# Kernel optimization log

Measured on AMD Instinct MI355X. Metric: run time of the kernel, lower is better.

Reference implementation:

```python
import math
import jax, jax.numpy as jnp
import numpy as np

B, T, E, H, D = 4, 2048, 1024, 16, 64


def make_pe(max_len, d_model):
    pos = np.arange(max_len, dtype=np.float32)[:, None]
    div = np.exp(np.arange(0, d_model, 2, dtype=np.float32) * (-math.log(10000.0) / d_model))
    pe = np.zeros((max_len, d_model), dtype=np.float32)
    pe[:, 0::2] = np.sin(pos * div)
    pe[:, 1::2] = np.cos(pos * div)
    return jnp.asarray(pe)


def _rel_shift(x):
    # x: [T, K, B, H] -- Transformer-XL relative shift
    Tq, K, b, h = x.shape
    zp = jnp.zeros((Tq, 1, b, h), x.dtype)
    xp = jnp.concatenate([zp, x], axis=1).reshape(K + 1, Tq, b, h)
    return xp[1:].reshape(Tq, K, b, h)


def setup_inputs() -> dict:
    key = jax.random.key(0)
    ks = jax.random.split(key, 7)
    word_embedding = jax.random.normal(ks[0], (B, T, E), dtype=jnp.float32)
    lens = jax.random.randint(ks[1], (B,), 128, T + 1)  # >=128 so no empty softmax rows
    # torch Linear weights are [out, in]
    Wqkv = jax.random.normal(ks[2], (3 * H * D, E), dtype=jnp.float32) * (1.0 / math.sqrt(E))
    Wpos = jax.random.normal(ks[3], (H * D, E), dtype=jnp.float32) * (1.0 / math.sqrt(E))
    Wout = jax.random.normal(ks[4], (E, H * D), dtype=jnp.float32) * (1.0 / math.sqrt(H * D))
    bound = math.sqrt(6.0 / (H + D))  # xavier_uniform on [H, D]
    r_w_bias = jax.random.uniform(ks[5], (H, D), minval=-bound, maxval=bound, dtype=jnp.float32)
    r_r_bias = jax.random.uniform(ks[6], (H, D), minval=-bound, maxval=bound, dtype=jnp.float32)
    return {"word_embedding": word_embedding, "lens": lens, "Wqkv": Wqkv,
            "Wpos": Wpos, "Wout": Wout, "r_w_bias": r_w_bias, "r_r_bias": r_r_bias}


def reference(word_embedding, lens, Wqkv, Wpos, Wout, r_w_bias, r_r_bias):
    scale = 1.0 / math.sqrt(D)
    we = jnp.transpose(word_embedding, (1, 0, 2))  # [T, B, E]
    K = T  # mems=None
    pe = make_pe(K, E)  # [K, E], constant buffer

    heads = jnp.einsum('tbe,fe->tbf', we, Wqkv)  # [T, B, 3HD]
    q, k, v = jnp.split(heads, 3, axis=-1)
    q = q.reshape(T, B, H, D)
    k = k.reshape(K, B, H, D)
    v = v.reshape(K, B, H, D)
    Rk = (pe @ Wpos.T).reshape(K, H, D)  # [K, H, D]

    AC = jnp.einsum('ibnd,jbnd->ijbn', q + r_w_bias, k)   # [T, K, B, H]
    BD = _rel_shift(jnp.einsum('ibnd,jnd->ijbn', q + r_r_bias, Rk))
    score = (AC + BD) * scale

    # mask: key position j invalid if j >= lens[b]
    mask = jnp.arange(K)[:, None] >= lens[None, :]       # [K, B]
    score = jnp.where(mask[None, :, :, None], -1e30, score)
    prob = jax.nn.softmax(score, axis=1)

    vec = jnp.einsum('ijbn,jbnd->ibnd', prob, v).reshape(T, B, H * D)
    out = jnp.einsum('tbf,ef->tbe', vec, Wout)           # [T, B, E]
    return jnp.transpose(out, (1, 0, 2))                 # [B, T, E]
```

## Files before the change

kernel.cpp:

```cpp
#include <hip/hip_runtime.h>
#include <hip/hip_bf16.h>
#include <math.h>
#include <stdint.h>

constexpr int Bc  = 4;
constexpr int Tc  = 2048;
constexpr int Ec  = 1024;
constexpr int Hc  = 16;
constexpr int Dc  = 64;
constexpr int HDc = Hc * Dc;
constexpr int Kc  = Tc;
constexpr float SCL2E = 0.18033688011112042f;

typedef __bf16 bf16;
typedef __attribute__((ext_vector_type(8))) __bf16 bf16x8;
typedef __attribute__((ext_vector_type(4))) __bf16 bf16x4;
typedef __attribute__((ext_vector_type(4))) float f32x4;
typedef __attribute__((ext_vector_type(4))) _Float16 f16x4;

__device__ __forceinline__ void gload16(const bf16* gp, bf16* lp) {
  __builtin_amdgcn_global_load_lds(
      (const __attribute__((address_space(1))) void*)gp,
      (__attribute__((address_space(3))) void*)lp, 16, 0, 0);
}

__global__ __launch_bounds__(256) void split_kernel(
    const float* __restrict__ src, bf16* __restrict__ hi,
    bf16* __restrict__ lo, int n) {
  int i = (blockIdx.x * 256 + threadIdx.x) * 4;
  if (i >= n) return;
  float4 v = *(const float4*)(src + i);
  bf16 h0 = (bf16)v.x, h1 = (bf16)v.y, h2 = (bf16)v.z, h3 = (bf16)v.w;
  bf16x4 H = {h0, h1, h2, h3};
  bf16x4 L = {(bf16)(v.x - (float)h0), (bf16)(v.y - (float)h1),
              (bf16)(v.z - (float)h2), (bf16)(v.w - (float)h3)};
  *(bf16x4*)(hi + i) = H;
  *(bf16x4*)(lo + i) = L;
}

__global__ __launch_bounds__(256) void round_kernel(
    const float* __restrict__ src, bf16* __restrict__ dst, int n) {
  int i = (blockIdx.x * 256 + threadIdx.x) * 4;
  if (i >= n) return;
  float4 v = *(const float4*)(src + i);
  bf16x4 H = {(bf16)v.x, (bf16)v.y, (bf16)v.z, (bf16)v.w};
  *(bf16x4*)(dst + i) = H;
}

__global__ __launch_bounds__(256) void pe_kernel(bf16* __restrict__ peH) {
  int idx = blockIdx.x * blockDim.x + threadIdx.x;
  if (idx >= Kc * (Ec / 2)) return;
  int r = idx / (Ec / 2);
  int i = idx % (Ec / 2);
  float div = __expf((float)i * -0.017988946039015984f);
  float ang = (float)r * div;
  size_t o = (size_t)r * Ec + 2 * i;
  peH[o]     = (bf16)sinf(ang);
  peH[o + 1] = (bf16)cosf(ang);
}

template <int EPI, int SPLIT>
__global__ __launch_bounds__(256) void gemm_mfma(
    const bf16* __restrict__ Ah_g, const bf16* __restrict__ Al_g,
    const bf16* __restrict__ Bh_g, const bf16* __restrict__ Bl_g,
    void* __restrict__ o0, void* __restrict__ o1,
    void* __restrict__ o2, void* __restrict__ o3,
    const float* __restrict__ rwb, const float* __restrict__ rrb,
    int Kd) {
  const int bn = blockIdx.x * 128, bm = blockIdx.y * 128;
  const int tid = threadIdx.x, wv = tid >> 6, lane = tid & 63;
  const int wm = wv >> 1, wn = wv & 1;
  const int g = lane >> 4, laneL = lane & 15;

  __shared__ bf16 lds[(SPLIT ? 4 : 2) * 128 * 64];
  bf16* Ah = lds;
  bf16* Al = lds + 8192;
  bf16* Bh = lds + (SPLIT ? 16384 : 8192);
  bf16* Bl = lds + 24576;

  f32x4 acc[4][4];
#pragma unroll
  for (int fi = 0; fi < 4; fi++)
#pragma unroll
    for (int fj = 0; fj < 4; fj++) acc[fi][fj] = (f32x4){0.f, 0.f, 0.f, 0.f};

  const int rb  = lane >> 3;
  const int cb8 = ((lane & 7) ^ rb) * 8;
  const bf16* Abase_h = Ah_g + (size_t)bm * Kd;
  const bf16* Abase_l = SPLIT ? Al_g + (size_t)bm * Kd : nullptr;
  const bf16* Bbase_h = Bh_g + (size_t)bn * Kd;
  const bf16* Bbase_l = SPLIT ? Bl_g + (size_t)bn * Kd : nullptr;

  for (int k0 = 0; k0 < Kd; k0 += 64) {
    __syncthreads();
#pragma unroll
    for (int t = 0; t < 4; t++) {
      int r = t * 32 + wv * 8 + rb;
      size_t go = (size_t)r * Kd + k0 + cb8;
      int lo_ = (t * 32 + wv * 8) * 64;
      gload16(Abase_h + go, Ah + lo_);
      gload16(Bbase_h + go, Bh + lo_);
      if (SPLIT) {
        gload16(Abase_l + go, Al + lo_);
        gload16(Bbase_l + go, Bl + lo_);
      }
    }
    __syncthreads();
#pragma unroll
    for (int kk = 0; kk < 2; kk++) {
      bf16x8 afh[4], afl[4], bfh[4], bfl[4];
#pragma unroll
      for (int fi = 0; fi < 4; fi++) {
        int row = wm * 64 + fi * 16 + laneL;
        int off = row * 64 + (((kk * 4 + g) ^ (row & 7)) * 8);
        afh[fi] = *(const bf16x8*)(Ah + off);
        if (SPLIT) afl[fi] = *(const bf16x8*)(Al + off);
      }
#pragma unroll
      for (int fj = 0; fj < 4; fj++) {
        int row = wn * 64 + fj * 16 + laneL;
        int off = row * 64 + (((kk * 4 + g) ^ (row & 7)) * 8);
        bfh[fj] = *(const bf16x8*)(Bh + off);
        if (SPLIT) bfl[fj] = *(const bf16x8*)(Bl + off);
      }
#pragma unroll
      for (int fi = 0; fi < 4; fi++)
#pragma unroll
        for (int fj = 0; fj < 4; fj++) {
          acc[fi][fj] = __builtin_amdgcn_mfma_f32_16x16x32_bf16(afh[fi], bfh[fj], acc[fi][fj], 0, 0, 0);
          if (SPLIT) {
            acc[fi][fj] = __builtin_amdgcn_mfma_f32_16x16x32_bf16(afh[fi], bfl[fj], acc[fi][fj], 0, 0, 0);
            acc[fi][fj] = __builtin_amdgcn_mfma_f32_16x16x32_bf16(afl[fi], bfh[fj], acc[fi][fj], 0, 0, 0);
          }
        }
    }
  }

#pragma unroll
  for (int fi = 0; fi < 4; fi++) {
#pragma unroll
    for (int fj = 0; fj < 4; fj++) {
      int n = bn + wn * 64 + fj * 16 + laneL;
      int sec = n >> 10, f = n & 1023, hh = f >> 6, d = f & 63;
      float rw = 0.f, rr = 0.f;
      if (EPI == 0 && sec == 0) { rw = rwb[f]; rr = rrb[f]; }
#pragma unroll
      for (int rg = 0; rg < 4; rg++) {
        int m = bm + wm * 64 + fi * 16 + g * 4 + rg;
        float cv = acc[fi][fj][rg];
        if (EPI == 0) {
          int bb = m >> 11, t = m & 2047;
          if (sec == 0) {
            size_t o = (((size_t)(bb * Hc + hh)) * Tc + t) * 64 + d;
            ((bf16*)o0)[o] = (bf16)((cv + rw) * SCL2E);
            ((bf16*)o1)[o] = (bf16)((cv + rr) * SCL2E);
          } else if (sec == 1) {
            ((bf16*)o2)[(((size_t)(bb * Hc + hh)) * Tc + t) * 64 + d] = (bf16)cv;
          } else {
            ((bf16*)o3)[(((size_t)(bb * Hc + hh)) * 64 + d) * Tc + t] = (bf16)cv;
          }
        } else if (EPI == 1) {
          ((bf16*)o0)[((size_t)(n >> 6) * Kc + m) * 64 + (n & 63)] = (bf16)cv;
        } else {
          ((float*)o0)[(size_t)m * 1024 + n] = cv;
        }
      }
    }
  }
}

__global__ __launch_bounds__(256, 2) void attn_mfma(
    const bf16* __restrict__ qw, const bf16* __restrict__ qr,
    const bf16* __restrict__ kbuf, const bf16* __restrict__ vT,
    const bf16* __restrict__ Rk, const int* __restrict__ lens,
    bf16* __restrict__ vecH, bf16* __restrict__ vecL) {
  const int bid = blockIdx.x;
  const int h  = (bid & 7) * 2 + ((bid >> 3) & 1);
  const int i0 = ((bid >> 4) & 31) * 64;
  const int b  = bid >> 9;
  const int tid = threadIdx.x, wv = tid >> 6, lane = tid & 63;
  const int g = lane >> 4, laneL = lane & 15;
  const int len = lens[b];

  __shared__ __attribute__((aligned(16))) _Float16 Gs[4][16 * 84];
  __shared__ bf16 Kst[2][64 * 64];
  __shared__ bf16 Vst[2][64 * 64];

  const size_t bh = (size_t)(b * Hc + h) * Tc * 64;
  const bf16* qwB = qw   + bh;
  const bf16* qrB = qr   + bh;
  const bf16* kB  = kbuf + bh;
  const bf16* vTB = vT   + bh;
  const bf16* RkB = Rk   + (size_t)h * Kc * 64;

  const int myrow  = i0 + wv * 16 + laneL;
  const int myrow2 = (myrow + 1 < Tc) ? myrow + 1 : Tc - 1;
  bf16x8 bqw[2], bq1[2], bq2[2];
#pragma unroll
  for (int kk = 0; kk < 2; kk++) {
    bqw[kk] = *(const bf16x8*)(qwB + (size_t)myrow  * 64 + kk * 32 + g * 8);
    bq1[kk] = *(const bf16x8*)(qrB + (size_t)myrow  * 64 + kk * 32 + g * 8);
    bq2[kk] = *(const bf16x8*)(qrB + (size_t)myrow2 * 64 + kk * 32 + g * 8);
  }

  float m_ = -1e30f, l_ = 0.f;
  f32x4 O[4];
#pragma unroll
  for (int nf = 0; nf < 4; nf++) O[nf] = (f32x4){0.f, 0.f, 0.f, 0.f};

  _Float16* Gp = &Gs[wv][0];
  bf16*     Pp = (bf16*)&Gs[wv][0];
  const int pswz = (laneL & 7) << 3;

  auto stage = [&](int buf, int j0n) __attribute__((always_inline)) {
#pragma unroll
    for (int t = 0; t < 2; t++) {
      const int r0  = wv * 16 + t * 8;
      const int row = r0 + (lane >> 3);
      const int c8  = (lane & 7) ^ ((lane >> 3) & 7);
      gload16(kB  + (size_t)(j0n + row) * 64 + c8 * 8, &Kst[buf][r0 * 64]);
      gload16(vTB + (size_t)row * Tc + j0n + c8 * 8,   &Vst[buf][r0 * 64]);
    }
  };

  auto issue_rk = [&](bf16x8 (&rf)[10], int j0n) __attribute__((always_inline)) {
    const int cn = i0 - j0n;
    const int pb = (cn >= 0 ? Tc - 16 - cn : -cn - 17) - wv * 16;
#pragma unroll
    for (int mf = 0; mf < 5; mf++) {
      int p = pb + mf * 16 + laneL;
      p = p < 0 ? 0 : (p > Kc - 1 ? Kc - 1 : p);
#pragma unroll
      for (int kk = 0; kk < 2; kk++)
        rf[mf * 2 + kk] = *(const bf16x8*)(RkB + (size_t)p * 64 + kk * 32 + g * 8);
    }
  };

  auto compute_tile = [&](int cur, int j0c, const bf16x8 (&rf)[10])
      __attribute__((always_inline)) {
    const int c = i0 - j0c;
    const int swz8 = laneL & 7;

    f32x4 ST[4];
    __builtin_amdgcn_s_setprio(1);
#pragma unroll
    for (int nf = 0; nf < 4; nf++) {
      f32x4 acc = (f32x4){0.f, 0.f, 0.f, 0.f};
#pragma unroll
      for (int kk = 0; kk < 2; kk++) {
        bf16x8 bk = *(const bf16x8*)(&Kst[cur][(nf * 16 + laneL) * 64 + (((kk * 4 + g) ^ swz8) * 8)]);
        acc = __builtin_amdgcn_mfma_f32_16x16x32_bf16(bk, bqw[kk], acc, 0, 0, 0);
      }
      ST[nf] = acc;
    }
    __builtin_amdgcn_s_setprio(0);

    const int iic  = wv * 16 + laneL + c;
    const int colb = laneL * 84 + 15 - laneL;
    float P_[4][4];

    if (c > 0) {
      __builtin_amdgcn_s_setprio(1);
#pragma unroll
      for (int mf = 0; mf < 5; mf++) {
        f32x4 acc = (f32x4){0.f, 0.f, 0.f, 0.f};
#pragma unroll
        for (int kk = 0; kk < 2; kk++)
          acc = __builtin_amdgcn_mfma_f32_16x16x32_bf16(rf[mf * 2 + kk], bq1[kk], acc, 0, 0, 0);
        f16x4 gv = {(_Float16)acc[0], (_Float16)acc[1], (_Float16)acc[2], (_Float16)acc[3]};
        *(f16x4*)(Gp + laneL * 84 + mf * 16 + g * 4) = gv;
      }
      __builtin_amdgcn_s_setprio(0);
#pragma unroll
      for (int nf = 0; nf < 4; nf++)
#pragma unroll
        for (int r = 0; r < 4; r++)
          P_[nf][r] = (float)Gp[colb + nf * 16 + g * 4 + r];
    } else if (c < 0) {
      __builtin_amdgcn_s_setprio(1);
#pragma unroll
      for (int mf = 0; mf < 5; mf++) {
        f32x4 acc = (f32x4){0.f, 0.f, 0.f, 0.f};
#pragma unroll
        for (int kk = 0; kk < 2; kk++)
          acc = __builtin_amdgcn_mfma_f32_16x16x32_bf16(rf[mf * 2 + kk], bq2[kk], acc, 0, 0, 0);
        f16x4 gv = {(_Float16)acc[0], (_Float16)acc[1], (_Float16)acc[2], (_Float16)acc[3]};
        *(f16x4*)(Gp + laneL * 84 + mf * 16 + g * 4) = gv;
      }
      __builtin_amdgcn_s_setprio(0);
#pragma unroll
      for (int nf = 0; nf < 4; nf++)
#pragma unroll
        for (int r = 0; r < 4; r++) {
          const int jj = nf * 16 + g * 4 + r;
          float g2v = (float)Gp[colb + jj];
          P_[nf][r] = (jj == iic + 1) ? 0.f : g2v;
        }
    } else {
      __builtin_amdgcn_s_setprio(1);
#pragma unroll
      for (int mf = 0; mf < 5; mf++) {
        f32x4 acc = (f32x4){0.f, 0.f, 0.f, 0.f};
#pragma unroll
        for (int kk = 0; kk < 2; kk++)
          acc = __builtin_amdgcn_mfma_f32_16x16x32_bf16(rf[mf * 2 + kk], bq1[kk], acc, 0, 0, 0);
        f16x4 gv = {(_Float16)acc[0], (_Float16)acc[1], (_Float16)acc[2], (_Float16)acc[3]};
        *(f16x4*)(Gp + laneL * 84 + mf * 16 + g * 4) = gv;
      }
      __builtin_amdgcn_s_setprio(0);
#pragma unroll
      for (int nf = 0; nf < 4; nf++)
#pragma unroll
        for (int r = 0; r < 4; r++)
          P_[nf][r] = (float)Gp[colb + nf * 16 + g * 4 + r];
      const int pb = -17 - wv * 16;
      __builtin_amdgcn_s_setprio(1);
#pragma unroll
      for (int mf = 0; mf < 5; mf++) {
        int p = pb + mf * 16 + laneL;
        p = p < 0 ? 0 : (p > Kc - 1 ? Kc - 1 : p);
        f32x4 acc = (f32x4){0.f, 0.f, 0.f, 0.f};
#pragma unroll
        for (int kk = 0; kk < 2; kk++) {
          bf16x8 ark = *(const bf16x8*)(RkB + (size_t)p * 64 + kk * 32 + g * 8);
          acc = __builtin_amdgcn_mfma_f32_16x16x32_bf16(ark, bq2[kk], acc, 0, 0, 0);
        }
        f16x4 gv = {(_Float16)acc[0], (_Float16)acc[1], (_Float16)acc[2], (_Float16)acc[3]};
        *(f16x4*)(Gp + laneL * 84 + mf * 16 + g * 4) = gv;
      }
      __builtin_amdgcn_s_setprio(0);
#pragma unroll
      for (int nf = 0; nf < 4; nf++)
#pragma unroll
        for (int r = 0; r < 4; r++) {
          const int jj = nf * 16 + g * 4 + r;
          float g2v = (float)Gp[colb + jj];
          P_[nf][r] = (jj <= iic) ? P_[nf][r] : ((jj == iic + 1) ? 0.f : g2v);
        }
    }

    float mx = -1e30f;
#pragma unroll
    for (int nf = 0; nf < 4; nf++)
#pragma unroll
      for (int r = 0; r < 4; r++) {
        float s = ST[nf][r] + P_[nf][r];
        P_[nf][r] = s;
        mx = fmaxf(mx, s);
      }
    if (j0c + 64 > len) {
#pragma unroll
      for (int nf = 0; nf < 4; nf++)
#pragma unroll
        for (int r = 0; r < 4; r++) {
          const int jj = nf * 16 + g * 4 + r;
          if (j0c + jj >= len) P_[nf][r] = -1e30f;
        }
      mx = -1e30f;
#pragma unroll
      for (int nf = 0; nf < 4; nf++)
#pragma unroll
        for (int r = 0; r < 4; r++) mx = fmaxf(mx, P_[nf][r]);
    }
    mx = fmaxf(mx, __shfl_xor(mx, 16));
    mx = fmaxf(mx, __shfl_xor(mx, 32));
    const float mnew = fmaxf(m_, mx);
    const bool norescale = __all(mnew == m_);
    const float fac = exp2f(m_ - mnew);
    float sum = 0.f;
#pragma unroll
    for (int nf = 0; nf < 4; nf++)
#pragma unroll
      for (int r = 0; r < 4; r++) {
        float p = exp2f(P_[nf][r] - mnew);
        P_[nf][r] = p;
        sum += p;
      }
    sum += __shfl_xor(sum, 16);
    sum += __shfl_xor(sum, 32);
    l_ = l_ * fac + sum;
    m_ = mnew;
    if (!norescale) {
#pragma unroll
      for (int nf = 0; nf < 4; nf++) O[nf] *= fac;
    }

    asm volatile("" ::: "memory");
#pragma unroll
    for (int mf = 0; mf < 4; mf++) {
      bf16x4 pv = {(bf16)P_[mf][0], (bf16)P_[mf][1], (bf16)P_[mf][2], (bf16)P_[mf][3]};
      *(bf16x4*)(Pp + laneL * 64 + ((mf * 16 + g * 4) ^ pswz)) = pv;
    }

    __builtin_amdgcn_s_setprio(1);
#pragma unroll
    for (int kk = 0; kk < 2; kk++) {
      bf16x8 pbf = *(const bf16x8*)(Pp + laneL * 64 + ((kk * 32 + g * 8) ^ pswz));
#pragma unroll
      for (int nf = 0; nf < 4; nf++) {
        bf16x8 av = *(const bf16x8*)(&Vst[cur][(nf * 16 + laneL) * 64 + (((kk * 4 + g) ^ swz8) * 8)]);
        O[nf] = __builtin_amdgcn_mfma_f32_16x16x32_bf16(av, pbf, O[nf], 0, 0, 0);
      }
    }
    __builtin_amdgcn_s_setprio(0);
  };

  auto cbar = [&]() __attribute__((always_inline)) {
    __builtin_amdgcn_sched_barrier(0);
    asm volatile("s_waitcnt vmcnt(10)" ::: "memory");
    __builtin_amdgcn_s_barrier();
    __builtin_amdgcn_sched_barrier(0);
  };

  const int ntiles = (len + 63) >> 6;
  bf16x8 rfA[10], rfB[10];
  issue_rk(rfA, 0);
  stage(0, 0);
  __syncthreads();
  int cur = 0;
  for (int t = 0; t < ntiles; t += 2) {
    const int j0 = t << 6;
    if (t + 1 < ntiles) {
      stage(cur ^ 1, j0 + 64);
      __builtin_amdgcn_sched_barrier(0);
      issue_rk(rfB, j0 + 64);
      compute_tile(cur, j0, rfA);
      cbar();
    } else {
      compute_tile(cur, j0, rfA);
      __syncthreads();
    }
    cur ^= 1;
    if (t + 1 < ntiles) {
      if (t + 2 < ntiles) {
        stage(cur ^ 1, j0 + 128);
        __builtin_amdgcn_sched_barrier(0);
        issue_rk(rfA, j0 + 128);
        compute_tile(cur, j0 + 64, rfB);
        cbar();
      } else {
        compute_tile(cur, j0 + 64, rfB);
        __syncthreads();
      }
      cur ^= 1;
    }
  }

  const float inv = 1.0f / l_;
  const size_t rowb = (size_t)(b * Tc + i0 + wv * 16 + laneL) * HDc + h * 64;
#pragma unroll
  for (int nf = 0; nf < 4; nf++) {
    float o0 = O[nf][0] * inv, o1 = O[nf][1] * inv,
          o2 = O[nf][2] * inv, o3 = O[nf][3] * inv;
    bf16x4 hv = {(bf16)o0, (bf16)o1, (bf16)o2, (bf16)o3};
    bf16x4 lv = {(bf16)(o0 - (float)hv[0]), (bf16)(o1 - (float)hv[1]),
                 (bf16)(o2 - (float)hv[2]), (bf16)(o3 - (float)hv[3])};
    *(bf16x4*)&vecH[rowb + nf * 16 + g * 4] = hv;
    *(bf16x4*)&vecL[rowb + nf * 16 + g * 4] = lv;
  }
}

extern "C" void kernel_launch(void* const* d_in, const int* in_sizes, int n_in,
                              void* d_out, int out_size, void* d_ws, size_t ws_size,
                              hipStream_t stream) {
  const float* we   = (const float*)d_in[0];
  const int*   lens = (const int*)  d_in[1];
  const float* Wqkv = (const float*)d_in[2];
  const float* Wpos = (const float*)d_in[3];
  const float* Wout = (const float*)d_in[4];
  const float* rwb  = (const float*)d_in[5];
  const float* rrb  = (const float*)d_in[6];
  float* out = (float*)d_out;

  bf16* ws = (bf16*)d_ws;
  const size_t BHTD = (size_t)Bc * Hc * Tc * Dc;
  bf16* qw    = ws;
  bf16* qr    = qw    + BHTD;
  bf16* kkp   = qr    + BHTD;
  bf16* vTp   = kkp   + BHTD;
  bf16* Rk    = vTp   + BHTD;
  bf16* peH   = Rk    + (size_t)Hc * Kc * Dc;
  bf16* weH   = peH   + (size_t)Kc * Ec;
  bf16* qkvH  = weH   + BHTD;
  bf16* WposH = qkvH  + (size_t)3 * HDc * Ec;
  bf16* WoutH = WposH + (size_t)HDc * Ec;
  bf16* WoutL = WoutH + (size_t)Ec * HDc;
  bf16* vecH  = WoutL + (size_t)Ec * HDc;
  bf16* vecL  = vecH  + BHTD;

  pe_kernel<<<(Kc * (Ec / 2) + 255) / 256, 256, 0, stream>>>(peH);
  round_kernel<<<(int)(BHTD / 1024), 256, 0, stream>>>(we, weH, (int)BHTD);
  round_kernel<<<3 * HDc * Ec / 1024, 256, 0, stream>>>(Wqkv, qkvH, 3 * HDc * Ec);
  round_kernel<<<HDc * Ec / 1024, 256, 0, stream>>>(Wpos, WposH, HDc * Ec);
  split_kernel<<<Ec * HDc / 1024, 256, 0, stream>>>(Wout, WoutH, WoutL, Ec * HDc);

  gemm_mfma<1, 0><<<dim3(HDc / 128, Kc / 128), 256, 0, stream>>>(
      peH, nullptr, WposH, nullptr, Rk, nullptr, nullptr, nullptr, nullptr, nullptr, Ec);
  gemm_mfma<0, 0><<<dim3(3 * HDc / 128, (Bc * Tc) / 128), 256, 0, stream>>>(
      weH, nullptr, qkvH, nullptr, qw, qr, kkp, vTp, rwb, rrb, Ec);
  attn_mfma<<<dim3(Tc / 64 * Hc * Bc), 256, 0, stream>>>(
      qw, qr, kkp, vTp, Rk, lens, vecH, vecL);
  gemm_mfma<2, 1><<<dim3(Ec / 128, (Bc * Tc) / 128), 256, 0, stream>>>(
      vecH, vecL, WoutH, WoutL, out, nullptr, nullptr, nullptr, nullptr, nullptr, HDc);
}
```

Measured before the change: 490.2 us.

## Triple-buffer K/V tiles in attention kernel to prefetch two tiles ahead

Expands the K/V shared-memory staging from double to triple buffering, so K/V loads are issued two tiles ahead of compute. Rk register loads are now issued before the K/V stage, and the vmcnt wait threshold is loosened to 14 when an extra stage is in flight. The goal is to hide more global-load latency behind the MFMA work. In exchange, LDS use per block grows by 16 KB, which may reduce occupancy against the launch bound of 2 blocks per CU.

```diff
diff --git a/kernel.cpp b/kernel.cpp
--- a/kernel.cpp
+++ b/kernel.cpp
@@ -183,8 +183,8 @@
   const int len = lens[b];
 
   __shared__ __attribute__((aligned(16))) _Float16 Gs[4][16 * 84];
-  __shared__ bf16 Kst[2][64 * 64];
-  __shared__ bf16 Vst[2][64 * 64];
+  __shared__ bf16 Kst[3][64 * 64];
+  __shared__ bf16 Vst[3][64 * 64];
 
   const size_t bh = (size_t)(b * Hc + h) * Tc * 64;
   const bf16* qwB = qw   + bh;
@@ -405,7 +405,13 @@
     __builtin_amdgcn_s_setprio(0);
   };
 
-  auto cbar = [&]() __attribute__((always_inline)) {
+  auto cbar14 = [&]() __attribute__((always_inline)) {
+    __builtin_amdgcn_sched_barrier(0);
+    asm volatile("s_waitcnt vmcnt(14)" ::: "memory");
+    __builtin_amdgcn_s_barrier();
+    __builtin_amdgcn_sched_barrier(0);
+  };
+  auto cbar10 = [&]() __attribute__((always_inline)) {
     __builtin_amdgcn_sched_barrier(0);
     asm volatile("s_waitcnt vmcnt(10)" ::: "memory");
     __builtin_amdgcn_s_barrier();
@@ -416,33 +422,36 @@
   bf16x8 rfA[10], rfB[10];
   issue_rk(rfA, 0);
   stage(0, 0);
+  stage(1, 64);
   __syncthreads();
-  int cur = 0;
+  int bc = 0;
   for (int t = 0; t < ntiles; t += 2) {
     const int j0 = t << 6;
     if (t + 1 < ntiles) {
-      stage(cur ^ 1, j0 + 64);
+      issue_rk(rfB, j0 + 64);
       __builtin_amdgcn_sched_barrier(0);
-      issue_rk(rfB, j0 + 64);
-      compute_tile(cur, j0, rfA);
-      cbar();
+      if (t + 2 < ntiles) { int b2 = bc == 0 ? 2 : bc - 1; stage(b2, j0 + 128); }
+      __builtin_amdgcn_sched_barrier(0);
+      compute_tile(bc, j0, rfA);
+      if (t + 2 < ntiles) cbar14(); else cbar10();
     } else {
-      compute_tile(cur, j0, rfA);
+      compute_tile(bc, j0, rfA);
       __syncthreads();
     }
-    cur ^= 1;
+    bc = bc == 2 ? 0 : bc + 1;
     if (t + 1 < ntiles) {
       if (t + 2 < ntiles) {
-        stage(cur ^ 1, j0 + 128);
+        issue_rk(rfA, j0 + 128);
         __builtin_amdgcn_sched_barrier(0);
-        issue_rk(rfA, j0 + 128);
-        compute_tile(cur, j0 + 64, rfB);
-        cbar();
+        if (t + 3 < ntiles) { int b3 = bc == 0 ? 2 : bc - 1; stage(b3, j0 + 192); }
+        __builtin_amdgcn_sched_barrier(0);
+        compute_tile(bc, j0 + 64, rfB);
+        if (t + 3 < ntiles) cbar14(); else cbar10();
       } else {
-        compute_tile(cur, j0 + 64, rfB);
+        compute_tile(bc, j0 + 64, rfB);
         __syncthreads();
       }
-      cur ^= 1;
+      bc = bc == 2 ? 0 : bc + 1;
     }
   }
 
```

Result: slower. 506.1 us (+3.2%).
